# Kernel tuning notes

Hardware: AMD Instinct MI355X
Metric: run time of the kernel (lower is better)

Reference implementation:

```python
import jax, jax.numpy as jnp
import numpy as np


def quat_to_rotmat(q):
    # q: [N,4] (w, x, y, z), normalized first (standard 3D-GS Transform)
    q = q / jnp.linalg.norm(q, axis=-1, keepdims=True)
    w, x, y, z = q[:, 0], q[:, 1], q[:, 2], q[:, 3]
    # rows of the 3x3 rotation matrix, stacked -> [N,3,3]
    r00 = 1 - 2 * (y * y + z * z)
    r01 = 2 * (x * y - w * z)
    r02 = 2 * (x * z + w * y)
    r10 = 2 * (x * y + w * z)
    r11 = 1 - 2 * (x * x + z * z)
    r12 = 2 * (y * z - w * x)
    r20 = 2 * (x * z - w * y)
    r21 = 2 * (y * z + w * x)
    r22 = 1 - 2 * (x * x + y * y)
    R = jnp.stack([
        jnp.stack([r00, r01, r02], axis=-1),
        jnp.stack([r10, r11, r12], axis=-1),
        jnp.stack([r20, r21, r22], axis=-1),
    ], axis=-2)
    return R


def setup_inputs() -> dict:
    key = jax.random.key(0)
    k1, k2 = jax.random.split(key)
    N = 4_000_000
    rotation = jax.random.normal(k1, (N, 4), dtype=jnp.float32)
    scale = jax.random.uniform(k2, (N, 3), dtype=jnp.float32)
    return {"rotation": rotation, "scale": scale}


def reference(rotation, scale):
    # get_covariance: M = R @ diag(scale); cov = M @ M^T  (symmetric PSD [N,3,3])
    R = quat_to_rotmat(rotation)          # [N,3,3]
    M = R * scale[:, None, :]             # R @ diag(scale), fused (no bmm)
    cov = jnp.einsum('nij,nkj->nik', M, M)  # M @ M^T
    return cov
```

## Files before the change

### kernel.cpp

```cpp
#include <hip/hip_runtime.h>


__global__ __launch_bounds__(256) void cov_main_kernel(
    const float4* __restrict__ rot4,
    const float4* __restrict__ scale4,
    float4* __restrict__ out4)
{
    __shared__ float s_scale[768];
    __shared__ __align__(16) float s_out[2304];
    const int t = threadIdx.x;
    const long long b = blockIdx.x;

    if (t < 192) {
        ((float4*)s_scale)[t] = scale4[b * 192 + t];
    }
    float4 q = rot4[b * 256 + t];
    __syncthreads();

    const float s0 = s_scale[t * 3 + 0];
    const float s1 = s_scale[t * 3 + 1];
    const float s2 = s_scale[t * 3 + 2];

    const float invn = rsqrtf(q.x * q.x + q.y * q.y + q.z * q.z + q.w * q.w);
    const float w = q.x * invn, x = q.y * invn, y = q.z * invn, z = q.w * invn;

    const float r00 = 1.f - 2.f * (y * y + z * z);
    const float r01 = 2.f * (x * y - w * z);
    const float r02 = 2.f * (x * z + w * y);
    const float r10 = 2.f * (x * y + w * z);
    const float r11 = 1.f - 2.f * (x * x + z * z);
    const float r12 = 2.f * (y * z - w * x);
    const float r20 = 2.f * (x * z - w * y);
    const float r21 = 2.f * (y * z + w * x);
    const float r22 = 1.f - 2.f * (x * x + y * y);

    const float m00 = r00 * s0, m01 = r01 * s1, m02 = r02 * s2;
    const float m10 = r10 * s0, m11 = r11 * s1, m12 = r12 * s2;
    const float m20 = r20 * s0, m21 = r21 * s1, m22 = r22 * s2;

    const float c00 = m00 * m00 + m01 * m01 + m02 * m02;
    const float c01 = m00 * m10 + m01 * m11 + m02 * m12;
    const float c02 = m00 * m20 + m01 * m21 + m02 * m22;
    const float c11 = m10 * m10 + m11 * m11 + m12 * m12;
    const float c12 = m10 * m20 + m11 * m21 + m12 * m22;
    const float c22 = m20 * m20 + m21 * m21 + m22 * m22;

    float* so = &s_out[t * 9];
    so[0] = c00; so[1] = c01; so[2] = c02;
    so[3] = c01; so[4] = c11; so[5] = c12;
    so[6] = c02; so[7] = c12; so[8] = c22;
    __syncthreads();

    const float4* sv = (const float4*)s_out;
    float4* ob = out4 + b * 576;
    ob[t]       = sv[t];
    ob[t + 256] = sv[t + 256];
    if (t < 64) ob[t + 512] = sv[t + 512];
}

__global__ void cov_tail_kernel(
    const float* __restrict__ rot,
    const float* __restrict__ scale,
    float* __restrict__ out,
    int start, int n)
{
    int i = start + blockIdx.x * blockDim.x + threadIdx.x;
    if (i >= n) return;
    const float qw = rot[i * 4 + 0], qx = rot[i * 4 + 1];
    const float qy = rot[i * 4 + 2], qz = rot[i * 4 + 3];
    const float s0 = scale[i * 3 + 0], s1 = scale[i * 3 + 1], s2 = scale[i * 3 + 2];
    const float invn = rsqrtf(qw * qw + qx * qx + qy * qy + qz * qz);
    const float w = qw * invn, x = qx * invn, y = qy * invn, z = qz * invn;
    const float r00 = 1.f - 2.f * (y * y + z * z);
    const float r01 = 2.f * (x * y - w * z);
    const float r02 = 2.f * (x * z + w * y);
    const float r10 = 2.f * (x * y + w * z);
    const float r11 = 1.f - 2.f * (x * x + z * z);
    const float r12 = 2.f * (y * z - w * x);
    const float r20 = 2.f * (x * z - w * y);
    const float r21 = 2.f * (y * z + w * x);
    const float r22 = 1.f - 2.f * (x * x + y * y);
    const float m00 = r00 * s0, m01 = r01 * s1, m02 = r02 * s2;
    const float m10 = r10 * s0, m11 = r11 * s1, m12 = r12 * s2;
    const float m20 = r20 * s0, m21 = r21 * s1, m22 = r22 * s2;
    float* o = out + (size_t)i * 9;
    o[0] = m00 * m00 + m01 * m01 + m02 * m02;
    o[1] = m00 * m10 + m01 * m11 + m02 * m12;
    o[2] = m00 * m20 + m01 * m21 + m02 * m22;
    o[3] = o[1];
    o[4] = m10 * m10 + m11 * m11 + m12 * m12;
    o[5] = m10 * m20 + m11 * m21 + m12 * m22;
    o[6] = o[2];
    o[7] = o[5];
    o[8] = m20 * m20 + m21 * m21 + m22 * m22;
}

extern "C" void kernel_launch(void* const* d_in, const int* in_sizes, int n_in,
                              void* d_out, int out_size, void* d_ws, size_t ws_size,
                              hipStream_t stream) {
    const float* rot   = (const float*)d_in[0];
    const float* scale = (const float*)d_in[1];
    float* out = (float*)d_out;

    const int N = in_sizes[0] / 4;
    const int nfull = N / 256;
    const int rem_start = nfull * 256;
    const int rem = N - rem_start;

    if (nfull > 0) {
        cov_main_kernel<<<nfull, 256, 0, stream>>>(
            (const float4*)rot, (const float4*)scale, (float4*)out);
    }
    if (rem > 0) {
        cov_tail_kernel<<<(rem + 255) / 256, 256, 0, stream>>>(
            rot, scale, out, rem_start, N);
    }
}
```

Measured before the change: 226.6 us.

## Process four Gaussians per thread with direct vectorized global loads and stores

Replaces the shared-memory staged block kernel with a kernel where each thread handles four Gaussians, loading four quaternions and three scale float4s directly and writing nine float4 outputs. This removes LDS staging and the two barriers. In exchange, per-lane global accesses become strided (144-byte output stride across lanes), so coalescing may suffer. Common math is factored into a shared device function.

```diff
diff --git a/kernel.cpp b/kernel.cpp
--- a/kernel.cpp
+++ b/kernel.cpp
@@ -1,26 +1,9 @@
 #include <hip/hip_runtime.h>
 
 
-__global__ __launch_bounds__(256) void cov_main_kernel(
-    const float4* __restrict__ rot4,
-    const float4* __restrict__ scale4,
-    float4* __restrict__ out4)
+__device__ __forceinline__ void cov_one(const float4 q, const float s0, const float s1,
+                                        const float s2, float* __restrict__ o)
 {
-    __shared__ float s_scale[768];
-    __shared__ __align__(16) float s_out[2304];
-    const int t = threadIdx.x;
-    const long long b = blockIdx.x;
-
-    if (t < 192) {
-        ((float4*)s_scale)[t] = scale4[b * 192 + t];
-    }
-    float4 q = rot4[b * 256 + t];
-    __syncthreads();
-
-    const float s0 = s_scale[t * 3 + 0];
-    const float s1 = s_scale[t * 3 + 1];
-    const float s2 = s_scale[t * 3 + 2];
-
     const float invn = rsqrtf(q.x * q.x + q.y * q.y + q.z * q.z + q.w * q.w);
     const float w = q.x * invn, x = q.y * invn, y = q.z * invn, z = q.w * invn;
 
@@ -45,17 +28,39 @@
     const float c12 = m10 * m20 + m11 * m21 + m12 * m22;
     const float c22 = m20 * m20 + m21 * m21 + m22 * m22;
 
-    float* so = &s_out[t * 9];
-    so[0] = c00; so[1] = c01; so[2] = c02;
-    so[3] = c01; so[4] = c11; so[5] = c12;
-    so[6] = c02; so[7] = c12; so[8] = c22;
-    __syncthreads();
+    o[0] = c00; o[1] = c01; o[2] = c02;
+    o[3] = c01; o[4] = c11; o[5] = c12;
+    o[6] = c02; o[7] = c12; o[8] = c22;
+}
 
-    const float4* sv = (const float4*)s_out;
-    float4* ob = out4 + b * 576;
-    ob[t]       = sv[t];
-    ob[t + 256] = sv[t + 256];
-    if (t < 64) ob[t + 512] = sv[t + 512];
+__global__ __launch_bounds__(256) void cov4_kernel(
+    const float4* __restrict__ rot4,
+    const float4* __restrict__ scale4,
+    float4* __restrict__ out4,
+    int nq)
+{
+    const int i = blockIdx.x * 256 + threadIdx.x;
+    if (i >= nq) return;
+
+    const size_t ib = (size_t)i;
+    const float4 q0 = rot4[ib * 4 + 0];
+    const float4 q1 = rot4[ib * 4 + 1];
+    const float4 q2 = rot4[ib * 4 + 2];
+    const float4 q3 = rot4[ib * 4 + 3];
+    const float4 sA = scale4[ib * 3 + 0];
+    const float4 sB = scale4[ib * 3 + 1];
+    const float4 sC = scale4[ib * 3 + 2];
+
+    __align__(16) float o[36];
+    cov_one(q0, sA.x, sA.y, sA.z, o + 0);
+    cov_one(q1, sA.w, sB.x, sB.y, o + 9);
+    cov_one(q2, sB.z, sB.w, sC.x, o + 18);
+    cov_one(q3, sC.y, sC.z, sC.w, o + 27);
+
+    const float4* ov = (const float4*)o;
+    float4* ob = out4 + ib * 9;
+#pragma unroll
+    for (int k = 0; k < 9; ++k) ob[k] = ov[k];
 }
 
 __global__ void cov_tail_kernel(
@@ -66,33 +71,12 @@
 {
     int i = start + blockIdx.x * blockDim.x + threadIdx.x;
     if (i >= n) return;
-    const float qw = rot[i * 4 + 0], qx = rot[i * 4 + 1];
-    const float qy = rot[i * 4 + 2], qz = rot[i * 4 + 3];
-    const float s0 = scale[i * 3 + 0], s1 = scale[i * 3 + 1], s2 = scale[i * 3 + 2];
-    const float invn = rsqrtf(qw * qw + qx * qx + qy * qy + qz * qz);
-    const float w = qw * invn, x = qx * invn, y = qy * invn, z = qz * invn;
-    const float r00 = 1.f - 2.f * (y * y + z * z);
-    const float r01 = 2.f * (x * y - w * z);
-    const float r02 = 2.f * (x * z + w * y);
-    const float r10 = 2.f * (x * y + w * z);
-    const float r11 = 1.f - 2.f * (x * x + z * z);
-    const float r12 = 2.f * (y * z - w * x);
-    const float r20 = 2.f * (x * z - w * y);
-    const float r21 = 2.f * (y * z + w * x);
-    const float r22 = 1.f - 2.f * (x * x + y * y);
-    const float m00 = r00 * s0, m01 = r01 * s1, m02 = r02 * s2;
-    const float m10 = r10 * s0, m11 = r11 * s1, m12 = r12 * s2;
-    const float m20 = r20 * s0, m21 = r21 * s1, m22 = r22 * s2;
-    float* o = out + (size_t)i * 9;
-    o[0] = m00 * m00 + m01 * m01 + m02 * m02;
-    o[1] = m00 * m10 + m01 * m11 + m02 * m12;
-    o[2] = m00 * m20 + m01 * m21 + m02 * m22;
-    o[3] = o[1];
-    o[4] = m10 * m10 + m11 * m11 + m12 * m12;
-    o[5] = m10 * m20 + m11 * m21 + m12 * m22;
-    o[6] = o[2];
-    o[7] = o[5];
-    o[8] = m20 * m20 + m21 * m21 + m22 * m22;
+    const float4 q = make_float4(rot[i * 4 + 0], rot[i * 4 + 1], rot[i * 4 + 2], rot[i * 4 + 3]);
+    float o[9];
+    cov_one(q, scale[i * 3 + 0], scale[i * 3 + 1], scale[i * 3 + 2], o);
+    float* dst = out + (size_t)i * 9;
+#pragma unroll
+    for (int k = 0; k < 9; ++k) dst[k] = o[k];
 }
 
 extern "C" void kernel_launch(void* const* d_in, const int* in_sizes, int n_in,
@@ -102,14 +86,14 @@
     const float* scale = (const float*)d_in[1];
     float* out = (float*)d_out;
 
-    const int N = in_sizes[0] / 4;
-    const int nfull = N / 256;
-    const int rem_start = nfull * 256;
+    const int N  = in_sizes[0] / 4;
+    const int nq = N / 4;
+    const int rem_start = nq * 4;
     const int rem = N - rem_start;
 
-    if (nfull > 0) {
-        cov_main_kernel<<<nfull, 256, 0, stream>>>(
-            (const float4*)rot, (const float4*)scale, (float4*)out);
+    if (nq > 0) {
+        cov4_kernel<<<(nq + 255) / 256, 256, 0, stream>>>(
+            (const float4*)rot, (const float4*)scale, (float4*)out, nq);
     }
     if (rem > 0) {
         cov_tail_kernel<<<(rem + 255) / 256, 256, 0, stream>>>(
```

Result: slower. 259.9 us (+14.7%).
